# Performance work log

Measured on AMD Instinct MI355X. Metric: run time of the kernel, lower is better.

## Reference

```python
import jax, jax.numpy as jnp
import numpy as np

B, S, E, H = 1024, 64, 1024, 16  # batch, seq (n_agent+1), n_embd, num_heads
D = E // H  # head_dim = 64


def setup_inputs() -> dict:
    k = jax.random.key(0)
    ks = jax.random.split(k, 7)
    w = lambda i: jax.random.normal(ks[i], (E, E), jnp.float32) * 0.02
    return {
        "query": jax.random.normal(ks[0], (B, S, E), jnp.float32),
        "key": jax.random.normal(ks[1], (B, S, E), jnp.float32),
        "value": jax.random.normal(ks[2], (B, S, E), jnp.float32),
        "Wq": w(3), "bq": jnp.zeros((E,), jnp.float32),
        "Wk": w(4), "bk": jnp.zeros((E,), jnp.float32),
        "Wv": w(5), "bv": jnp.zeros((E,), jnp.float32),
        "Wo": w(6), "bo": jnp.zeros((E,), jnp.float32),
    }


def reference(query, key, value, Wq, bq, Wk, bk, Wv, bv, Wo, bo):
    Bq, Q, _ = query.shape
    K = key.shape[1]
    # projections -> [B, H, L, D]
    q = (query @ Wq + bq).reshape(Bq, Q, H, D).transpose(0, 2, 1, 3)
    k = (key @ Wk + bk).reshape(Bq, K, H, D).transpose(0, 2, 1, 3)
    v = (value @ Wv + bv).reshape(Bq, K, H, D).transpose(0, 2, 1, 3)
    # non-standard: ReLU on Q and K before scores
    q = jnp.maximum(q, 0.0)
    k = jnp.maximum(k, 0.0)
    scale = 1.0 / jnp.sqrt(jnp.float32(D))
    scores = jnp.einsum('bhqd,bhkd->bhqk', q, k) * scale  # [B,H,Q,K]
    # causal mask (tril of the (n_agent+1)^2 mask, sliced to q_len,kv_len)
    mask = jnp.tril(jnp.ones((Q, K), jnp.float32))[None, None]
    scores = jnp.where(mask == 0, jnp.finfo(jnp.float32).min, scores)
    attn = jax.nn.softmax(scores, axis=-1)
    out = jnp.einsum('bhqk,bhkd->bhqd', attn, v)
    out = out.transpose(0, 2, 1, 3).reshape(Bq, Q, E)
    return out @ Wo + bo
```

## Files before the change

kernel.cpp:

```cpp
#include <hip/hip_runtime.h>

typedef __attribute__((ext_vector_type(4))) float f32x4;
typedef __attribute__((ext_vector_type(8))) short short8;
typedef __attribute__((ext_vector_type(2))) unsigned int uint2v;
typedef __attribute__((ext_vector_type(4))) unsigned int uint4v;

#define MFMA_BF16(a,b,c) __builtin_amdgcn_mfma_f32_16x16x32_bf16(a,b,c,0,0,0)

__device__ __forceinline__ unsigned short bf16_of(float f) {
  union { float f; unsigned int u; } v; v.f = f;
  unsigned int r = v.u + 0x7fffu + ((v.u >> 16) & 1u);
  return (unsigned short)(r >> 16);
}

__device__ __forceinline__ unsigned int cvt_pk_bf16(float lo, float hi) {
  unsigned int r;
  asm("v_cvt_pk_bf16_f32 %0, %1, %2" : "=v"(r) : "v"(lo), "v"(hi));
  return r;
}

__device__ __forceinline__ void gload_lds16(const void* g, void* l) {
  __builtin_amdgcn_global_load_lds(
      (const __attribute__((address_space(1))) unsigned int*)g,
      (__attribute__((address_space(3))) unsigned int*)l, 16, 0, 0);
}

__global__ __launch_bounds__(256)
void wcast_kernel(const float* __restrict__ W0, const float* __restrict__ W1,
                  const float* __restrict__ W2, const float* __restrict__ W3,
                  unsigned short* __restrict__ wt) {
  __shared__ float tile[64][65];
  const float* W = (blockIdx.z == 0) ? W0 : (blockIdx.z == 1) ? W1
                 : (blockIdx.z == 2) ? W2 : W3;
  unsigned short* Wt = wt + (size_t)blockIdx.z * (1024u * 1024u);
  int k0 = blockIdx.x * 64, n0 = blockIdx.y * 64;
  int t = threadIdx.x, r = t >> 6, c = t & 63;
#pragma unroll
  for (int i = 0; i < 16; ++i)
    tile[r + i * 4][c] = W[(size_t)(k0 + r + i * 4) * 1024 + n0 + c];
  __syncthreads();
#pragma unroll
  for (int i = 0; i < 16; ++i)
    Wt[(size_t)(n0 + r + i * 4) * 1024 + k0 + c] = bf16_of(tile[c][r + i * 4]);
}

template <int MODE>
__global__ __launch_bounds__(512, 4)
void gemm_kernel(const void* __restrict__ A_, const unsigned short* __restrict__ Bt,
                 const float* __restrict__ bias, void* __restrict__ C_) {
  constexpr bool AF32 = (MODE != 2);
  __shared__ unsigned short ldsA[128 * 64];
  __shared__ unsigned short ldsB[256 * 64];

  int bid = blockIdx.x;
  int mt = (bid & 7) * 64 + (bid >> 5);
  int nt = (bid >> 3) & 3;
  int m0 = mt * 128, n0 = nt * 256;

  int tid = threadIdx.x;
  int w = tid >> 6, l = tid & 63;
  int wm = w >> 2, wn = w & 3;
  int li = l & 15, grp = l >> 4;

  f32x4 acc[4][4] = {};

  const float* Af = (const float*)A_;
  const unsigned short* Ab = (const unsigned short*)A_;

  int grow = l >> 3;
  int gseg = (l & 7) ^ grow;

  int rA = tid >> 2, q = tid & 3;

  f32x4 areg[4];
  if constexpr (AF32) {
#pragma unroll
    for (int j = 0; j < 4; ++j)
      areg[j] = *(const f32x4*)(Af + (size_t)(m0 + rA) * 1024 + q * 16 + j * 4);
  }

  for (int kt = 0; kt < 16; ++kt) {
    int k0 = kt * 64;
    if constexpr (AF32) {
      uint4v w0, w1;
      w0[0] = cvt_pk_bf16(areg[0][0], areg[0][1]);
      w0[1] = cvt_pk_bf16(areg[0][2], areg[0][3]);
      w0[2] = cvt_pk_bf16(areg[1][0], areg[1][1]);
      w0[3] = cvt_pk_bf16(areg[1][2], areg[1][3]);
      w1[0] = cvt_pk_bf16(areg[2][0], areg[2][1]);
      w1[1] = cvt_pk_bf16(areg[2][2], areg[2][3]);
      w1[2] = cvt_pk_bf16(areg[3][0], areg[3][1]);
      w1[3] = cvt_pk_bf16(areg[3][2], areg[3][3]);
      *(uint4v*)((char*)ldsA + rA * 128 + (((2 * q)     ^ (rA & 7)) << 4)) = w0;
      *(uint4v*)((char*)ldsA + rA * 128 + (((2 * q + 1) ^ (rA & 7)) << 4)) = w1;
    } else {
#pragma unroll
      for (int i = 0; i < 2; ++i) {
        int c = w * 2 + i;
        gload_lds16(Ab + (size_t)(m0 + 8 * c + grow) * 1024 + k0 + gseg * 8,
                    (char*)ldsA + c * 1024);
      }
    }
#pragma unroll
    for (int i = 0; i < 4; ++i) {
      int c = w * 4 + i;
      gload_lds16(Bt + (size_t)(n0 + 8 * c + grow) * 1024 + k0 + gseg * 8,
                  (char*)ldsB + c * 1024);
    }
    if constexpr (AF32) {
      if (kt < 15) {
#pragma unroll
        for (int j = 0; j < 4; ++j)
          areg[j] = *(const f32x4*)(Af + (size_t)(m0 + rA) * 1024 + (k0 + 64) + q * 16 + j * 4);
      }
    }
    __syncthreads();
#pragma unroll
    for (int ks = 0; ks < 2; ++ks) {
      short8 af[4], bf[4];
#pragma unroll
      for (int mi = 0; mi < 4; ++mi) {
        int row = wm * 64 + mi * 16 + li;
        af[mi] = *(const short8*)((const char*)ldsA + row * 128 +
                                  (((ks * 4 + grp) ^ (row & 7)) << 4));
      }
#pragma unroll
      for (int ni = 0; ni < 4; ++ni) {
        int row = wn * 64 + ni * 16 + li;
        bf[ni] = *(const short8*)((const char*)ldsB + row * 128 +
                                  (((ks * 4 + grp) ^ (row & 7)) << 4));
      }
#pragma unroll
      for (int mi = 0; mi < 4; ++mi)
#pragma unroll
        for (int ni = 0; ni < 4; ++ni)
          acc[mi][ni] = MFMA_BF16(af[mi], bf[ni], acc[mi][ni]);
    }
    __syncthreads();
  }

  int mrow0 = m0 + wm * 64;
  int ncol0 = n0 + wn * 64;
  float bvv[4];
#pragma unroll
  for (int ni = 0; ni < 4; ++ni) bvv[ni] = bias[ncol0 + ni * 16 + li];

  if constexpr (MODE == 2) {
    float* C = (float*)C_;
#pragma unroll
    for (int mi = 0; mi < 4; ++mi)
#pragma unroll
      for (int ni = 0; ni < 4; ++ni)
#pragma unroll
        for (int j = 0; j < 4; ++j)
          C[(size_t)(mrow0 + mi * 16 + grp * 4 + j) * 1024 + ncol0 + ni * 16 + li] =
              acc[mi][ni][j] + bvv[ni];
  } else if constexpr (MODE == 0) {
    unsigned short* C = (unsigned short*)C_;
    int b = mrow0 >> 6, h = ncol0 >> 6;
    unsigned short* base = C + (size_t)b * 65536 + (size_t)h * 4096;
#pragma unroll
    for (int mi = 0; mi < 4; ++mi)
#pragma unroll
      for (int ni = 0; ni < 4; ++ni)
#pragma unroll
        for (int j = 0; j < 4; ++j) {
          float v = acc[mi][ni][j] + bvv[ni];
          v = fmaxf(v, 0.0f);
          base[(mi * 16 + grp * 4 + j) * 64 + ni * 16 + li] = bf16_of(v);
        }
  } else {
    unsigned short* C = (unsigned short*)C_;
    int b = mrow0 >> 6, h = ncol0 >> 6;
    unsigned short* base = C + (size_t)b * 65536 + (size_t)h * 4096;
#pragma unroll
    for (int mi = 0; mi < 4; ++mi)
#pragma unroll
      for (int ni = 0; ni < 4; ++ni) {
        uint2v pk;
        pk.x = cvt_pk_bf16(acc[mi][ni][0] + bvv[ni], acc[mi][ni][1] + bvv[ni]);
        pk.y = cvt_pk_bf16(acc[mi][ni][2] + bvv[ni], acc[mi][ni][3] + bvv[ni]);
        *(uint2v*)(base + (ni * 16 + li) * 64 + mi * 16 + grp * 4) = pk;
      }
  }
}

__global__ __launch_bounds__(64)
void attn_kernel(const unsigned short* __restrict__ qw,
                 const unsigned short* __restrict__ kw,
                 const unsigned short* __restrict__ vw,
                 unsigned short* __restrict__ aw) {
  __shared__ unsigned short p_lds[64 * 72];
  int bh = blockIdx.x;
  int b = bh >> 4, h = bh & 15;
  int l = threadIdx.x;
  int li = l & 15, grp = l >> 4;
  const unsigned short* qb = qw + (size_t)bh * 4096;
  const unsigned short* kb = kw + (size_t)bh * 4096;
  const unsigned short* vb = vw + (size_t)bh * 4096;

  short8 aq[4][2], bk_[4][2];
#pragma unroll
  for (int mi = 0; mi < 4; ++mi)
#pragma unroll
    for (int ks = 0; ks < 2; ++ks) {
      aq[mi][ks]  = *(const short8*)(qb + (mi * 16 + li) * 64 + ks * 32 + grp * 8);
      bk_[mi][ks] = *(const short8*)(kb + (mi * 16 + li) * 64 + ks * 32 + grp * 8);
    }

  f32x4 sf[4][4];
#pragma unroll
  for (int mi = 0; mi < 4; ++mi)
#pragma unroll
    for (int ni = 0; ni < 4; ++ni) {
      f32x4 t = {};
      t = MFMA_BF16(aq[mi][0], bk_[ni][0], t);
      t = MFMA_BF16(aq[mi][1], bk_[ni][1], t);
      sf[mi][ni] = t;
    }

#pragma unroll
  for (int mi = 0; mi < 4; ++mi) {
#pragma unroll
    for (int j = 0; j < 4; ++j) {
      int row = mi * 16 + grp * 4 + j;
      float mx = -1e30f;
#pragma unroll
      for (int ni = 0; ni < 4; ++ni) {
        int col = ni * 16 + li;
        float v = sf[mi][ni][j] * 0.125f;
        v = (col <= row) ? v : -1e30f;
        sf[mi][ni][j] = v;
        mx = fmaxf(mx, v);
      }
#pragma unroll
      for (int sh = 1; sh < 16; sh <<= 1) mx = fmaxf(mx, __shfl_xor(mx, sh, 64));
      float sum = 0.0f;
#pragma unroll
      for (int ni = 0; ni < 4; ++ni) {
        float e = __expf(sf[mi][ni][j] - mx);
        sf[mi][ni][j] = e;
        sum += e;
      }
#pragma unroll
      for (int sh = 1; sh < 16; sh <<= 1) sum += __shfl_xor(sum, sh, 64);
      float rr = 1.0f / sum;
#pragma unroll
      for (int ni = 0; ni < 4; ++ni) sf[mi][ni][j] *= rr;
    }
  }

#pragma unroll
  for (int mi = 0; mi < 4; ++mi)
#pragma unroll
    for (int ni = 0; ni < 4; ++ni)
#pragma unroll
      for (int j = 0; j < 4; ++j)
        p_lds[(mi * 16 + grp * 4 + j) * 72 + ni * 16 + li] = bf16_of(sf[mi][ni][j]);
  __syncthreads();

  short8 pa[4][2], bv_[4][2];
#pragma unroll
  for (int mi = 0; mi < 4; ++mi)
#pragma unroll
    for (int ks = 0; ks < 2; ++ks)
      pa[mi][ks] = *(const short8*)(p_lds + (mi * 16 + li) * 72 + ks * 32 + grp * 8);
#pragma unroll
  for (int ni = 0; ni < 4; ++ni)
#pragma unroll
    for (int ks = 0; ks < 2; ++ks)
      bv_[ni][ks] = *(const short8*)(vb + (ni * 16 + li) * 64 + ks * 32 + grp * 8);

  f32x4 of[4][4];
#pragma unroll
  for (int mi = 0; mi < 4; ++mi)
#pragma unroll
    for (int ni = 0; ni < 4; ++ni) {
      f32x4 t = {};
      t = MFMA_BF16(pa[mi][0], bv_[ni][0], t);
      t = MFMA_BF16(pa[mi][1], bv_[ni][1], t);
      of[mi][ni] = t;
    }

  unsigned short* ab = aw + (size_t)b * 65536 + (size_t)h * 64;
#pragma unroll
  for (int mi = 0; mi < 4; ++mi)
#pragma unroll
    for (int ni = 0; ni < 4; ++ni)
#pragma unroll
      for (int j = 0; j < 4; ++j)
        ab[(size_t)(mi * 16 + grp * 4 + j) * 1024 + ni * 16 + li] = bf16_of(of[mi][ni][j]);
}

extern "C" void kernel_launch(void* const* d_in, const int* in_sizes, int n_in,
                              void* d_out, int out_size, void* d_ws, size_t ws_size,
                              hipStream_t stream) {
  (void)in_sizes; (void)n_in; (void)out_size; (void)ws_size;
  const float* query = (const float*)d_in[0];
  const float* key   = (const float*)d_in[1];
  const float* value = (const float*)d_in[2];
  const float* Wq = (const float*)d_in[3];
  const float* bq = (const float*)d_in[4];
  const float* Wk = (const float*)d_in[5];
  const float* bk = (const float*)d_in[6];
  const float* Wv = (const float*)d_in[7];
  const float* bv = (const float*)d_in[8];
  const float* Wo = (const float*)d_in[9];
  const float* bo = (const float*)d_in[10];
  float* out = (float*)d_out;

  unsigned short* wt = (unsigned short*)d_ws;
  const size_t NE = (size_t)67108864;
  unsigned short* qw = wt + (size_t)4 * 1024 * 1024;
  unsigned short* kw = qw + NE;
  unsigned short* vw = kw + NE;
  unsigned short* aw = vw + NE;

  wcast_kernel<<<dim3(16, 16, 4), 256, 0, stream>>>(Wq, Wk, Wv, Wo, wt);
  gemm_kernel<0><<<dim3(2048), 512, 0, stream>>>(query, wt + (size_t)0 * 1048576, bq, qw);
  gemm_kernel<0><<<dim3(2048), 512, 0, stream>>>(key,   wt + (size_t)1 * 1048576, bk, kw);
  gemm_kernel<1><<<dim3(2048), 512, 0, stream>>>(value, wt + (size_t)2 * 1048576, bv, vw);
  attn_kernel<<<dim3(16384), 64, 0, stream>>>(qw, kw, vw, aw);
  gemm_kernel<2><<<dim3(2048), 512, 0, stream>>>(aw, wt + (size_t)3 * 1048576, bo, out);
}
```

Measured before the change: 923.3 us.

## Merge QKV projections into one launch and double-buffer the output GEMM

The three Q/K/V projection GEMMs now run as a single launch, using blockIdx.z to select the input, weight, bias and output, so they can fill the GPU together and two launch gaps disappear. The output projection becomes its own kernel with 128x128 tiles, 256 threads and double-buffered LDS, so global-to-LDS loads for the next K tile overlap the MFMA work on the current one. The z-based selection adds a runtime branch in the epilogue. Doubling the LDS buffers and changing the tile shape can alter occupancy.

```diff
diff --git a/kernel.cpp b/kernel.cpp
--- a/kernel.cpp
+++ b/kernel.cpp
@@ -44,13 +44,20 @@
     Wt[(size_t)(n0 + r + i * 4) * 1024 + k0 + c] = bf16_of(tile[c][r + i * 4]);
 }
 
-template <int MODE>
 __global__ __launch_bounds__(512, 4)
-void gemm_kernel(const void* __restrict__ A_, const unsigned short* __restrict__ Bt,
-                 const float* __restrict__ bias, void* __restrict__ C_) {
-  constexpr bool AF32 = (MODE != 2);
+void gemm_qkv(const float* __restrict__ Aq, const float* __restrict__ Ak,
+              const float* __restrict__ Av, const unsigned short* __restrict__ wt,
+              const float* __restrict__ bq, const float* __restrict__ bk,
+              const float* __restrict__ bv, unsigned short* __restrict__ qw,
+              unsigned short* __restrict__ kw, unsigned short* __restrict__ vw) {
   __shared__ unsigned short ldsA[128 * 64];
   __shared__ unsigned short ldsB[256 * 64];
+
+  int z = blockIdx.z;
+  const float* Af = (z == 0) ? Aq : (z == 1) ? Ak : Av;
+  const unsigned short* Bt = wt + (size_t)z * 1048576;
+  const float* bias = (z == 0) ? bq : (z == 1) ? bk : bv;
+  unsigned short* C = (z == 0) ? qw : (z == 1) ? kw : vw;
 
   int bid = blockIdx.x;
   int mt = (bid & 7) * 64 + (bid >> 5);
@@ -64,24 +71,19 @@
 
   f32x4 acc[4][4] = {};
 
-  const float* Af = (const float*)A_;
-  const unsigned short* Ab = (const unsigned short*)A_;
-
   int grow = l >> 3;
   int gseg = (l & 7) ^ grow;
 
   int rA = tid >> 2, q = tid & 3;
 
   f32x4 areg[4];
-  if constexpr (AF32) {
-#pragma unroll
-    for (int j = 0; j < 4; ++j)
-      areg[j] = *(const f32x4*)(Af + (size_t)(m0 + rA) * 1024 + q * 16 + j * 4);
-  }
+#pragma unroll
+  for (int j = 0; j < 4; ++j)
+    areg[j] = *(const f32x4*)(Af + (size_t)(m0 + rA) * 1024 + q * 16 + j * 4);
 
   for (int kt = 0; kt < 16; ++kt) {
     int k0 = kt * 64;
-    if constexpr (AF32) {
+    {
       uint4v w0, w1;
       w0[0] = cvt_pk_bf16(areg[0][0], areg[0][1]);
       w0[1] = cvt_pk_bf16(areg[0][2], areg[0][3]);
@@ -93,13 +95,6 @@
       w1[3] = cvt_pk_bf16(areg[3][2], areg[3][3]);
       *(uint4v*)((char*)ldsA + rA * 128 + (((2 * q)     ^ (rA & 7)) << 4)) = w0;
       *(uint4v*)((char*)ldsA + rA * 128 + (((2 * q + 1) ^ (rA & 7)) << 4)) = w1;
-    } else {
-#pragma unroll
-      for (int i = 0; i < 2; ++i) {
-        int c = w * 2 + i;
-        gload_lds16(Ab + (size_t)(m0 + 8 * c + grow) * 1024 + k0 + gseg * 8,
-                    (char*)ldsA + c * 1024);
-      }
     }
 #pragma unroll
     for (int i = 0; i < 4; ++i) {
@@ -107,12 +102,10 @@
       gload_lds16(Bt + (size_t)(n0 + 8 * c + grow) * 1024 + k0 + gseg * 8,
                   (char*)ldsB + c * 1024);
     }
-    if constexpr (AF32) {
-      if (kt < 15) {
-#pragma unroll
-        for (int j = 0; j < 4; ++j)
-          areg[j] = *(const f32x4*)(Af + (size_t)(m0 + rA) * 1024 + (k0 + 64) + q * 16 + j * 4);
-      }
+    if (kt < 15) {
+#pragma unroll
+      for (int j = 0; j < 4; ++j)
+        areg[j] = *(const f32x4*)(Af + (size_t)(m0 + rA) * 1024 + (k0 + 64) + q * 16 + j * 4);
     }
     __syncthreads();
 #pragma unroll
@@ -145,20 +138,9 @@
 #pragma unroll
   for (int ni = 0; ni < 4; ++ni) bvv[ni] = bias[ncol0 + ni * 16 + li];
 
-  if constexpr (MODE == 2) {
-    float* C = (float*)C_;
-#pragma unroll
-    for (int mi = 0; mi < 4; ++mi)
-#pragma unroll
-      for (int ni = 0; ni < 4; ++ni)
-#pragma unroll
-        for (int j = 0; j < 4; ++j)
-          C[(size_t)(mrow0 + mi * 16 + grp * 4 + j) * 1024 + ncol0 + ni * 16 + li] =
-              acc[mi][ni][j] + bvv[ni];
-  } else if constexpr (MODE == 0) {
-    unsigned short* C = (unsigned short*)C_;
-    int b = mrow0 >> 6, h = ncol0 >> 6;
-    unsigned short* base = C + (size_t)b * 65536 + (size_t)h * 4096;
+  int b = mrow0 >> 6, h = ncol0 >> 6;
+  unsigned short* base = C + (size_t)b * 65536 + (size_t)h * 4096;
+  if (z < 2) {
 #pragma unroll
     for (int mi = 0; mi < 4; ++mi)
 #pragma unroll
@@ -170,9 +152,6 @@
           base[(mi * 16 + grp * 4 + j) * 64 + ni * 16 + li] = bf16_of(v);
         }
   } else {
-    unsigned short* C = (unsigned short*)C_;
-    int b = mrow0 >> 6, h = ncol0 >> 6;
-    unsigned short* base = C + (size_t)b * 65536 + (size_t)h * 4096;
 #pragma unroll
     for (int mi = 0; mi < 4; ++mi)
 #pragma unroll
@@ -183,6 +162,90 @@
         *(uint2v*)(base + (ni * 16 + li) * 64 + mi * 16 + grp * 4) = pk;
       }
   }
+}
+
+__global__ __launch_bounds__(256, 4)
+void gemm_out(const unsigned short* __restrict__ Ab, const unsigned short* __restrict__ Bt,
+              const float* __restrict__ bias, float* __restrict__ C) {
+  __shared__ unsigned short ldsA[2][128 * 64];
+  __shared__ unsigned short ldsB[2][128 * 64];
+
+  int bid = blockIdx.x;
+  int mt = (bid & 7) * 64 + (bid >> 6);
+  int nt = (bid >> 3) & 7;
+  int m0 = mt * 128, n0 = nt * 128;
+
+  int tid = threadIdx.x;
+  int w = tid >> 6, l = tid & 63;
+  int wm = w >> 1, wn = w & 1;
+  int li = l & 15, grp = l >> 4;
+
+  f32x4 acc[4][4] = {};
+
+  int grow = l >> 3;
+  int gseg = (l & 7) ^ grow;
+
+  auto stage = [&](int buf, int kt) {
+#pragma unroll
+    for (int i = 0; i < 4; ++i) {
+      int c = w * 4 + i;
+      gload_lds16(Ab + (size_t)(m0 + 8 * c + grow) * 1024 + kt * 64 + gseg * 8,
+                  (char*)&ldsA[buf][0] + c * 1024);
+    }
+#pragma unroll
+    for (int i = 0; i < 4; ++i) {
+      int c = w * 4 + i;
+      gload_lds16(Bt + (size_t)(n0 + 8 * c + grow) * 1024 + kt * 64 + gseg * 8,
+                  (char*)&ldsB[buf][0] + c * 1024);
+    }
+  };
+
+  stage(0, 0);
+  __syncthreads();
+
+  for (int kt = 0; kt < 16; ++kt) {
+    int cur = kt & 1;
+    if (kt < 15) {
+      stage(cur ^ 1, kt + 1);
+      __builtin_amdgcn_sched_barrier(0);
+    }
+#pragma unroll
+    for (int ks = 0; ks < 2; ++ks) {
+      short8 af[4], bf[4];
+#pragma unroll
+      for (int mi = 0; mi < 4; ++mi) {
+        int row = wm * 64 + mi * 16 + li;
+        af[mi] = *(const short8*)((const char*)&ldsA[cur][0] + row * 128 +
+                                  (((ks * 4 + grp) ^ (row & 7)) << 4));
+      }
+#pragma unroll
+      for (int ni = 0; ni < 4; ++ni) {
+        int row = wn * 64 + ni * 16 + li;
+        bf[ni] = *(const short8*)((const char*)&ldsB[cur][0] + row * 128 +
+                                  (((ks * 4 + grp) ^ (row & 7)) << 4));
+      }
+#pragma unroll
+      for (int mi = 0; mi < 4; ++mi)
+#pragma unroll
+        for (int ni = 0; ni < 4; ++ni)
+          acc[mi][ni] = MFMA_BF16(af[mi], bf[ni], acc[mi][ni]);
+    }
+    __syncthreads();
+  }
+
+  int mrow0 = m0 + wm * 64;
+  int ncol0 = n0 + wn * 64;
+  float bvv[4];
+#pragma unroll
+  for (int ni = 0; ni < 4; ++ni) bvv[ni] = bias[ncol0 + ni * 16 + li];
+#pragma unroll
+  for (int mi = 0; mi < 4; ++mi)
+#pragma unroll
+    for (int ni = 0; ni < 4; ++ni)
+#pragma unroll
+      for (int j = 0; j < 4; ++j)
+        C[(size_t)(mrow0 + mi * 16 + grp * 4 + j) * 1024 + ncol0 + ni * 16 + li] =
+            acc[mi][ni][j] + bvv[ni];
 }
 
 __global__ __launch_bounds__(64)
@@ -317,9 +380,8 @@
   unsigned short* aw = vw + NE;
 
   wcast_kernel<<<dim3(16, 16, 4), 256, 0, stream>>>(Wq, Wk, Wv, Wo, wt);
-  gemm_kernel<0><<<dim3(2048), 512, 0, stream>>>(query, wt + (size_t)0 * 1048576, bq, qw);
-  gemm_kernel<0><<<dim3(2048), 512, 0, stream>>>(key,   wt + (size_t)1 * 1048576, bk, kw);
-  gemm_kernel<1><<<dim3(2048), 512, 0, stream>>>(value, wt + (size_t)2 * 1048576, bv, vw);
+  gemm_qkv<<<dim3(2048, 1, 3), 512, 0, stream>>>(query, key, value, wt,
+                                                 bq, bk, bv, qw, kw, vw);
   attn_kernel<<<dim3(16384), 64, 0, stream>>>(qw, kw, vw, aw);
-  gemm_kernel<2><<<dim3(2048), 512, 0, stream>>>(aw, wt + (size_t)3 * 1048576, bo, out);
-}
+  gemm_out<<<dim3(4096), 256, 0, stream>>>(aw, wt + (size_t)3 * 1048576, bo, out);
+}
```

Result: slower. 968.3 us (+4.9%).
